# Optimization experiments

Hardware: AMD Instinct MI355X
Metric: run time of the kernel (lower is better)

## Reference

```python
import jax, jax.numpy as jnp
import numpy as np
import math

N = 8192
IN_FEATURES = 512
OUT_FEATURES = 512
BUCKET = 4          # self.bucket -> number of hash buckets
NHASH = 1           # nHashTable hardcoded to 1 in forward
NEG = -9e15         # sentinel used by the original module


def setup_inputs() -> dict:
    key = jax.random.key(0)
    k_in, k_adj, k_rot, k_kw, k_vw = jax.random.split(key, 5)
    inp = jax.random.normal(k_in, (N, IN_FEATURES), dtype=jnp.float32)
    adj = jax.random.randint(k_adj, (N, N), 0, 2, dtype=jnp.int32)
    rotations_rands = jax.random.normal(k_rot, (NHASH, OUT_FEATURES, BUCKET // 2), dtype=jnp.float32)
    # xavier_uniform with gain=1.414 for (in, out) matrices
    limit = 1.414 * math.sqrt(6.0 / (IN_FEATURES + OUT_FEATURES))
    kW = jax.random.uniform(k_kw, (IN_FEATURES, OUT_FEATURES), minval=-limit, maxval=limit, dtype=jnp.float32)
    vW = jax.random.uniform(k_vw, (IN_FEATURES, OUT_FEATURES), minval=-limit, maxval=limit, dtype=jnp.float32)
    return {"input": inp, "adj": adj, "rotations_rands": rotations_rands, "kW": kW, "vW": vW}


def reference(input, adj, rotations_rands, kW, vW):
    kh = input @ kW                      # [N, H]
    vh = input @ vW                      # [N, H]
    H = kh.shape[1]

    # LSH bucketing: rotate keys, argmax over [r, -r] -> bucket id per node
    rv = jnp.einsum('nh,thb->tnb', kh, rotations_rands)   # [1, N, B/2]
    rv = jnp.concatenate([rv, -rv], axis=-1)              # [1, N, B]
    buckets = jnp.argmax(rv, axis=2)[0]                   # [N]

    # Original scatters per-bucket kh@kh.T blocks into a dense NxN matrix
    # initialized at NEG; equivalent to masking full scores by same-bucket.
    same_bucket = buckets[:, None] == buckets[None, :]    # [N, N]
    scores = (kh @ kh.T) / jnp.sqrt(jnp.asarray(H, kh.dtype))
    K = jnp.where(same_bucket, scores, NEG)

    attention = jnp.where(adj > 0, K, NEG)
    attention = jax.nn.softmax(attention, axis=1)
    # dropout is identity in eval mode (reference runs in eval)
    h_prime = attention @ vh                              # [N, H]
    return jax.nn.elu(h_prime)                            # concat=True -> ELU
```

## Files before the change

kernel.cpp:

```cpp
#include <hip/hip_runtime.h>
#include <hip/hip_bf16.h>
#include <math.h>

#define N_NODES 8192
#define FEAT 512
#define NEGV -9e15f
#define VHPT_W 8704

typedef __attribute__((ext_vector_type(8))) short short8;
typedef __attribute__((ext_vector_type(4))) float floatx4;

#define OFF_KH    0UL
#define OFF_VH    16777216UL
#define OFF_KHP   33554432UL
#define OFF_VHPT  42074112UL
#define OFF_MASK  50987008UL
#define OFF_S     59375616UL
#define OFF_PERM  109707264UL
#define OFF_FLAGS 109740032UL
#define OFF_BUCK  109772800UL
#define OFF_META  109805568UL
#define OFF_CMEAN 109806592UL
#define WS_NEEDED 109808640UL
#define CAP_S     25165824L

#define OFF_AHI   (OFF_S)
#define OFF_ALO   (OFF_S + 8388608UL)
#define OFF_WKHI  (OFF_S + 16777216UL)
#define OFF_WKLO  (OFF_S + 17301504UL)
#define OFF_WVHI  (OFF_S + 17825792UL)
#define OFF_WVLO  (OFF_S + 18350080UL)
#define OFF_CW    (OFF_MASK)

static __device__ __forceinline__ unsigned short f2bf_bits(float x) {
  __hip_bfloat16 h = __float2bfloat16(x);
  unsigned short u;
  __builtin_memcpy(&u, &h, 2);
  return u;
}
static __device__ __forceinline__ float bf_bits2f(unsigned short u) {
  __hip_bfloat16 h;
  __builtin_memcpy(&h, &u, 2);
  return __bfloat162float(h);
}

static __device__ __forceinline__ void async_copy16(const void* gptr,
                                                    void* lptr) {
  __builtin_amdgcn_global_load_lds(
      (const __attribute__((address_space(1))) unsigned int*)gptr,
      (__attribute__((address_space(3))) unsigned int*)lptr, 16, 0, 0);
}

__global__ __launch_bounds__(256) void convert_input(
    const float* __restrict__ A, __hip_bfloat16* __restrict__ Ahi,
    __hip_bfloat16* __restrict__ Alo) {
  const long idx = ((long)blockIdx.x * 256 + threadIdx.x) * 4;
  const float4 v = *(const float4*)&A[idx];
  const float vv[4] = {v.x, v.y, v.z, v.w};
  ushort4 hi, lo;
  unsigned short* hp = (unsigned short*)&hi;
  unsigned short* lp = (unsigned short*)&lo;
#pragma unroll
  for (int e = 0; e < 4; e++) {
    unsigned short h = f2bf_bits(vv[e]);
    hp[e] = h;
    lp[e] = f2bf_bits(vv[e] - bf_bits2f(h));
  }
  *(ushort4*)&Ahi[idx] = hi;
  *(ushort4*)&Alo[idx] = lo;
}

__global__ __launch_bounds__(256) void convert_w(
    const float* __restrict__ kW, const float* __restrict__ vW,
    __hip_bfloat16* __restrict__ WkhiT, __hip_bfloat16* __restrict__ WkloT,
    __hip_bfloat16* __restrict__ WvhiT, __hip_bfloat16* __restrict__ WvloT) {
  __shared__ float tile[64][65];
  const int z = blockIdx.z;
  const float* __restrict__ W = z ? vW : kW;
  __hip_bfloat16* __restrict__ HiT = z ? WvhiT : WkhiT;
  __hip_bfloat16* __restrict__ LoT = z ? WvloT : WkloT;
  const int k0 = blockIdx.x * 64, n0 = blockIdx.y * 64;
  const int t = threadIdx.x;
#pragma unroll
  for (int s = 0; s < 16; s++) {
    int idx = t + s * 256;
    int r = idx >> 6, c = idx & 63;
    tile[r][c] = W[(long)(k0 + r) * FEAT + n0 + c];
  }
  __syncthreads();
#pragma unroll
  for (int s = 0; s < 16; s++) {
    int idx = t + s * 256;
    int a = idx >> 6, b = idx & 63;
    float w = tile[b][a];
    unsigned short h = f2bf_bits(w);
    unsigned short l = f2bf_bits(w - bf_bits2f(h));
    __builtin_memcpy(&HiT[(long)(n0 + a) * FEAT + k0 + b], &h, 2);
    __builtin_memcpy(&LoT[(long)(n0 + a) * FEAT + k0 + b], &l, 2);
  }
}

__global__ __launch_bounds__(256) void mfma_dual(
    const __hip_bfloat16* __restrict__ Ahi, const __hip_bfloat16* __restrict__ Alo,
    const __hip_bfloat16* __restrict__ WkhiT, const __hip_bfloat16* __restrict__ WkloT,
    const __hip_bfloat16* __restrict__ WvhiT, const __hip_bfloat16* __restrict__ WvloT,
    float* __restrict__ kh, float* __restrict__ vh) {
  const int z = blockIdx.z;
  const __hip_bfloat16* __restrict__ WhiT = z ? WvhiT : WkhiT;
  const __hip_bfloat16* __restrict__ WloT = z ? WvloT : WkloT;
  float* __restrict__ outp = z ? vh : kh;
  const int ti = blockIdx.x, tj = blockIdx.y;
  __shared__ __align__(16) __hip_bfloat16 Ah[128 * 32];
  __shared__ __align__(16) __hip_bfloat16 Al[128 * 32];
  __shared__ __align__(16) __hip_bfloat16 Wh[128 * 32];
  __shared__ __align__(16) __hip_bfloat16 Wl[128 * 32];
  const int t = threadIdx.x;
  const int lane = t & 63, w = t >> 6;
  const int wm = (w >> 1) * 64, wn = (w & 1) * 64;
  const int quad = lane >> 4, ln = lane & 15;
  const int qr = quad * 8;
  floatx4 acc[4][4];
#pragma unroll
  for (int mi = 0; mi < 4; mi++)
#pragma unroll
    for (int ni = 0; ni < 4; ni++) acc[mi][ni] = (floatx4)0.f;
  for (int k0 = 0; k0 < FEAT; k0 += 32) {
    __syncthreads();
#pragma unroll
    for (int s = 0; s < 2; s++) {
      int c = t + s * 256;
      int row = c >> 2, off8 = (c & 3) * 8;
      int lo = row * 32 + off8;
      async_copy16(&Ahi[(long)(ti * 128 + row) * FEAT + k0 + off8], &Ah[lo]);
      async_copy16(&Alo[(long)(ti * 128 + row) * FEAT + k0 + off8], &Al[lo]);
      async_copy16(&WhiT[(long)(tj * 128 + row) * FEAT + k0 + off8], &Wh[lo]);
      async_copy16(&WloT[(long)(tj * 128 + row) * FEAT + k0 + off8], &Wl[lo]);
    }
    __syncthreads();
    short8 ah[4], al[4], bh[4], bl[4];
#pragma unroll
    for (int mi = 0; mi < 4; mi++) {
      ah[mi] = *(const short8*)&Ah[(wm + mi * 16 + ln) * 32 + qr];
      al[mi] = *(const short8*)&Al[(wm + mi * 16 + ln) * 32 + qr];
    }
#pragma unroll
    for (int ni = 0; ni < 4; ni++) {
      bh[ni] = *(const short8*)&Wh[(wn + ni * 16 + ln) * 32 + qr];
      bl[ni] = *(const short8*)&Wl[(wn + ni * 16 + ln) * 32 + qr];
    }
#pragma unroll
    for (int mi = 0; mi < 4; mi++)
#pragma unroll
      for (int ni = 0; ni < 4; ni++) {
        acc[mi][ni] = __builtin_amdgcn_mfma_f32_16x16x32_bf16(
            ah[mi], bh[ni], acc[mi][ni], 0, 0, 0);
        acc[mi][ni] = __builtin_amdgcn_mfma_f32_16x16x32_bf16(
            ah[mi], bl[ni], acc[mi][ni], 0, 0, 0);
        acc[mi][ni] = __builtin_amdgcn_mfma_f32_16x16x32_bf16(
            al[mi], bh[ni], acc[mi][ni], 0, 0, 0);
      }
  }
#pragma unroll
  for (int mi = 0; mi < 4; mi++)
#pragma unroll
    for (int ni = 0; ni < 4; ni++) {
      int cc = tj * 128 + wn + ni * 16 + ln;
#pragma unroll
      for (int reg = 0; reg < 4; reg++) {
        int r = ti * 128 + wm + mi * 16 + quad * 4 + reg;
        outp[(long)r * FEAT + cc] = acc[mi][ni][reg];
      }
    }
}

__global__ __launch_bounds__(64) void cw_kernel(
    const float* __restrict__ kW, const float* __restrict__ rot,
    double* __restrict__ cw) {
  const int f = blockIdx.x;
  const int lane = threadIdx.x;
  double r0 = 0.0, r1 = 0.0;
  for (int h = lane; h < FEAT; h += 64) {
    double a = (double)kW[(long)f * FEAT + h];
    r0 += a * (double)rot[2 * h];
    r1 += a * (double)rot[2 * h + 1];
  }
#pragma unroll
  for (int off = 32; off > 0; off >>= 1) {
    r0 += __shfl_down(r0, off);
    r1 += __shfl_down(r1, off);
  }
  if (lane == 0) {
    cw[2 * f] = r0;
    cw[2 * f + 1] = r1;
  }
}

__global__ __launch_bounds__(64) void rv_bucket_kernel(
    const float* __restrict__ input, const double* __restrict__ cw,
    int* __restrict__ buckets) {
  const int i = blockIdx.x;
  const int lane = threadIdx.x;
  double r0 = 0.0, r1 = 0.0;
  for (int f = lane; f < FEAT; f += 64) {
    double a = (double)input[(long)i * FEAT + f];
    r0 += a * cw[2 * f];
    r1 += a * cw[2 * f + 1];
  }
#pragma unroll
  for (int off = 32; off > 0; off >>= 1) {
    r0 += __shfl_down(r0, off);
    r1 += __shfl_down(r1, off);
  }
  if (lane == 0) {
    int b = 0;
    double best = r0;
    if (r1 > best)  { best = r1;  b = 1; }
    if (-r0 > best) { best = -r0; b = 2; }
    if (-r1 > best) { best = -r1; b = 3; }
    buckets[i] = b;
  }
}

__global__ __launch_bounds__(256) void sort_kernel(
    const int* __restrict__ buckets, int* __restrict__ perm,
    int* __restrict__ meta, float* __restrict__ cmean) {
  __shared__ int lc[4][256];
  __shared__ int sc[4][256];
  __shared__ int boff_sh[5];
  const int t = threadIdx.x;
  cmean[t] = 0.f;
  cmean[t + 256] = 0.f;
  const int base = t * 32;
  int c0 = 0, c1 = 0, c2 = 0, c3 = 0;
  for (int k = 0; k < 32; k++) {
    int b = buckets[base + k];
    c0 += (b == 0); c1 += (b == 1); c2 += (b == 2); c3 += (b == 3);
  }
  lc[0][t] = c0; lc[1][t] = c1; lc[2][t] = c2; lc[3][t] = c3;
  sc[0][t] = c0; sc[1][t] = c1; sc[2][t] = c2; sc[3][t] = c3;
  __syncthreads();
  for (int off = 1; off < 256; off <<= 1) {
    int a0 = (t >= off) ? sc[0][t - off] : 0;
    int a1 = (t >= off) ? sc[1][t - off] : 0;
    int a2 = (t >= off) ? sc[2][t - off] : 0;
    int a3 = (t >= off) ? sc[3][t - off] : 0;
    __syncthreads();
    sc[0][t] += a0; sc[1][t] += a1; sc[2][t] += a2; sc[3][t] += a3;
    __syncthreads();
  }
  if (t == 0) {
    int boff[5];
    boff[0] = 0;
    for (int b = 0; b < 4; b++) boff[b + 1] = boff[b] + sc[b][255];
    for (int b = 0; b < 5; b++) { meta[b] = boff[b]; boff_sh[b] = boff[b]; }
    long so = 0;
    int po = 0;
    for (int b = 0; b < 4; b++) {
      int tot = boff[b + 1] - boff[b];
      int pad = ((tot + 127) >> 7) << 7;
      meta[5 + b] = pad;
      meta[9 + b] = (int)so;
      meta[14 + b] = po;
      so += (long)pad * pad;
      po += pad;
    }
    meta[13] = (int)so;
    meta[18] = po;
    if (so > CAP_S)
      for (int b = 0; b < 4; b++) meta[5 + b] = 0;
  }
  __syncthreads();
  int s0 = boff_sh[0] + sc[0][t] - lc[0][t];
  int s1 = boff_sh[1] + sc[1][t] - lc[1][t];
  int s2 = boff_sh[2] + sc[2][t] - lc[2][t];
  int s3 = boff_sh[3] + sc[3][t] - lc[3][t];
  for (int k = 0; k < 32; k++) {
    int i = base + k;
    int b = buckets[i];
    int pos = (b == 0) ? s0++ : ((b == 1) ? s1++ : ((b == 2) ? s2++ : s3++));
    perm[pos] = i;
  }
}

__global__ __launch_bounds__(256) void gather_khp_kernel(
    const float* __restrict__ kh, const int* __restrict__ perm,
    __hip_bfloat16* __restrict__ khp) {
  const int g = blockIdx.x;
  const int t = threadIdx.x;
  if (g < N_NODES) {
    const int p = perm[g];
    const float2 v = *(const float2*)&kh[(long)p * FEAT + 2 * t];
    khp[(long)g * FEAT + 2 * t] = __float2bfloat16(v.x);
    khp[(long)g * FEAT + 2 * t + 1] = __float2bfloat16(v.y);
  } else {
    khp[(long)g * FEAT + 2 * t] = __float2bfloat16(0.f);
    khp[(long)g * FEAT + 2 * t + 1] = __float2bfloat16(0.f);
  }
}

__global__ __launch_bounds__(256) void transpose_vhpT_kernel(
    const float* __restrict__ vh, const int* __restrict__ perm,
    const int* __restrict__ meta, __hip_bfloat16* __restrict__ vhpT,
    float* __restrict__ cmean) {
  __shared__ float tile[64][65];
  __shared__ float cred[4][64];
  const int g0 = blockIdx.x * 64;
  const int f0 = blockIdx.y * 64;
  const int t = threadIdx.x;
#pragma unroll
  for (int s = 0; s < 16; s++) {
    int idx = t + s * 256;
    int r = idx >> 6, c = idx & 63;
    int pos = g0 + r;
    int b = (pos >= meta[15]) + (pos >= meta[16]) + (pos >= meta[17]);
    int local = pos - meta[14 + b];
    int n_b = meta[b + 1] - meta[b];
    float v = 0.f;
    if (local < n_b) v = vh[(long)perm[meta[b] + local] * FEAT + f0 + c];
    tile[r][c] = v;
  }
  __syncthreads();
  {
    const int c = t & 63, seg = t >> 6;
    float ps = 0.f;
#pragma unroll
    for (int rr = 0; rr < 16; rr++) ps += tile[seg * 16 + rr][c];
    cred[seg][c] = ps;
  }
  __syncthreads();
  if (t < 64)
    atomicAdd(&cmean[f0 + t],
              cred[0][t] + cred[1][t] + cred[2][t] + cred[3][t]);
#pragma unroll
  for (int s = 0; s < 16; s++) {
    int idx = t + s * 256;
    int fr = idx >> 6, gc = idx & 63;
    vhpT[(long)(f0 + fr) * VHPT_W + g0 + gc] = __float2bfloat16(tile[gc][fr]);
  }
}

__global__ __launch_bounds__(256) void maskpack_kernel(
    const int* __restrict__ adj, const int* __restrict__ perm,
    const int* __restrict__ meta, unsigned long long* __restrict__ maskbits) {
  __shared__ int adj_lds[N_NODES];
  const int g = blockIdx.x;
  const int t = threadIdx.x;
  const int b = (g >= meta[1]) + (g >= meta[2]) + (g >= meta[3]);
  const int boff = meta[b];
  const int n_b = meta[b + 1] - boff;
  const int padded = meta[5 + b];
  const int i = perm[g];
  const int* arow = adj + (long)i * N_NODES;
#pragma unroll
  for (int s = 0; s < 8; s++) {
    int idx = (t + s * 256) * 4;
    *(int4*)&adj_lds[idx] = *(const int4*)&arow[idx];
  }
  __syncthreads();
  const int lane = t & 63, w = t >> 6;
  for (int jj0 = w * 64; jj0 < padded; jj0 += 256) {
    int jj = jj0 + lane;
    int pred = 0;
    if (jj < n_b) pred = adj_lds[perm[boff + jj]] > 0;
    unsigned long long mword = __ballot(pred);
    if (lane == 0) maskbits[(long)g * 128 + (jj0 >> 6)] = mword;
  }
}

__global__ __launch_bounds__(256) void s_gemm(
    const __hip_bfloat16* __restrict__ khp, const int* __restrict__ meta,
    const unsigned long long* __restrict__ maskbits,
    __hip_bfloat16* __restrict__ S) {
  const int b = blockIdx.z;
  const int padded = meta[5 + b];
  const int ti = blockIdx.x, tj = blockIdx.y;
  if (ti * 128 >= padded || tj * 128 >= padded) return;
  const int boff = meta[b];
  const long soff = meta[9 + b];
  __shared__ __align__(16) __hip_bfloat16 As[128 * 32];
  __shared__ __align__(16) __hip_bfloat16 Bs[128 * 32];
  const int t = threadIdx.x;
  const int lane = t & 63, w = t >> 6;
  const int wm = (w >> 1) * 64, wn = (w & 1) * 64;
  const int quad = lane >> 4, ln = lane & 15;
  const int qr = quad * 8;
  floatx4 acc[4][4];
#pragma unroll
  for (int mi = 0; mi < 4; mi++)
#pragma unroll
    for (int ni = 0; ni < 4; ni++) acc[mi][ni] = (floatx4)0.f;
  const long a_g0 = boff + ti * 128;
  const long b_g0 = boff + tj * 128;
  for (int k0 = 0; k0 < FEAT; k0 += 32) {
    __syncthreads();
#pragma unroll
    for (int s = 0; s < 2; s++) {
      int c = t + s * 256;
      int row = c >> 2, off8 = (c & 3) * 8;
      int lo = row * 32 + off8;
      async_copy16(&khp[(a_g0 + row) * FEAT + k0 + off8], &As[lo]);
      async_copy16(&khp[(b_g0 + row) * FEAT + k0 + off8], &Bs[lo]);
    }
    __syncthreads();
    short8 af[4], bfr[4];
#pragma unroll
    for (int mi = 0; mi < 4; mi++)
      af[mi] = *(const short8*)&As[(wm + mi * 16 + ln) * 32 + qr];
#pragma unroll
    for (int ni = 0; ni < 4; ni++)
      bfr[ni] = *(const short8*)&Bs[(wn + ni * 16 + ln) * 32 + qr];
#pragma unroll
    for (int mi = 0; mi < 4; mi++)
#pragma unroll
      for (int ni = 0; ni < 4; ni++)
        acc[mi][ni] = __builtin_amdgcn_mfma_f32_16x16x32_bf16(
            af[mi], bfr[ni], acc[mi][ni], 0, 0, 0);
  }
  const float scale = 0.04419417382415922f;
#pragma unroll
  for (int mi = 0; mi < 4; mi++) {
#pragma unroll
    for (int ni = 0; ni < 4; ni++) {
      int cb = tj * 128 + wn + ni * 16;
#pragma unroll
      for (int reg = 0; reg < 4; reg++) {
        int r = ti * 128 + wm + mi * 16 + quad * 4 + reg;
        unsigned long long wbits = maskbits[(long)(boff + r) * 128 + (cb >> 6)];
        int bit = (int)((wbits >> ((cb & 63) + ln)) & 1ULL);
        float v = acc[mi][ni][reg] * scale;
        S[soff + (long)r * padded + cb + ln] =
            __float2bfloat16(bit ? v : NEGV);
      }
    }
  }
}

__global__ __launch_bounds__(256) void softmax_kernel(
    __hip_bfloat16* __restrict__ S, const int* __restrict__ meta,
    int* __restrict__ flags) {
  const int g = blockIdx.x;
  const int b = (g >= meta[1]) + (g >= meta[2]) + (g >= meta[3]);
  const int boff = meta[b];
  const int padded = meta[5 + b];
  const long soff = meta[9 + b];
  __hip_bfloat16* row = S + soff + (long)(g - boff) * padded;
  __shared__ float red[256];
  __shared__ float pb[8192];
  const int t = threadIdx.x;
  float m = -INFINITY;
  for (int j0 = t * 8; j0 < padded; j0 += 2048) {
    union { short8 v; unsigned short u[8]; } pk;
    pk.v = *(const short8*)&row[j0];
#pragma unroll
    for (int e = 0; e < 8; e++) {
      float s = bf_bits2f(pk.u[e]);
      pb[j0 + e] = s;
      m = fmaxf(m, s);
    }
  }
  red[t] = m;
  __syncthreads();
#pragma unroll
  for (int o = 128; o > 0; o >>= 1) {
    if (t < o) red[t] = fmaxf(red[t], red[t + o]);
    __syncthreads();
  }
  m = red[0];
  __syncthreads();
  if (m < -8e15f) {
    if (t == 0) flags[g] = 1;
    union { short8 v; unsigned short u[8]; } zz;
#pragma unroll
    for (int e = 0; e < 8; e++) zz.u[e] = 0;
    for (int j0 = t * 8; j0 < padded; j0 += 2048) *(short8*)&row[j0] = zz.v;
    return;
  }
  if (t == 0) flags[g] = 0;
  float sum = 0.f;
  for (int j0 = t * 8; j0 < padded; j0 += 2048) {
#pragma unroll
    for (int e = 0; e < 8; e++) {
      float ex = expf(pb[j0 + e] - m);
      pb[j0 + e] = ex;
      sum += ex;
    }
  }
  red[t] = sum;
  __syncthreads();
#pragma unroll
  for (int o = 128; o > 0; o >>= 1) {
    if (t < o) red[t] += red[t + o];
    __syncthreads();
  }
  const float inv = 1.f / red[0];
  for (int j0 = t * 8; j0 < padded; j0 += 2048) {
    union { short8 v; unsigned short u[8]; } pk;
#pragma unroll
    for (int e = 0; e < 8; e++) pk.u[e] = f2bf_bits(pb[j0 + e] * inv);
    *(short8*)&row[j0] = pk.v;
  }
}

__global__ __launch_bounds__(256) void pv_gemm(
    const __hip_bfloat16* __restrict__ S, const __hip_bfloat16* __restrict__ vhpT,
    const int* __restrict__ meta, const int* __restrict__ perm,
    const int* __restrict__ flags, const float* __restrict__ cmean,
    float* __restrict__ out) {
  const int b = blockIdx.z;
  const int padded = meta[5 + b];
  const int ti = blockIdx.x;
  if (ti * 128 >= padded) return;
  const int boff = meta[b];
  const int n_b = meta[b + 1] - boff;
  const long soff = meta[9 + b];
  const int poff = meta[14 + b];
  const int f0 = blockIdx.y * 64;
  __shared__ __align__(16) __hip_bfloat16 As[128 * 32];
  __shared__ __align__(16) __hip_bfloat16 Bs[64 * 32];
  const int t = threadIdx.x;
  const int lane = t & 63, w = t >> 6;
  const int wm = w * 32;
  const int quad = lane >> 4, ln = lane & 15;
  const int qr = quad * 8;
  floatx4 acc[2][4];
#pragma unroll
  for (int mi = 0; mi < 2; mi++)
#pragma unroll
    for (int ni = 0; ni < 4; ni++) acc[mi][ni] = (floatx4)0.f;
  const long r0 = (long)ti * 128;
  for (int k0 = 0; k0 < padded; k0 += 32) {
    __syncthreads();
#pragma unroll
    for (int s = 0; s < 2; s++) {
      int c = t + s * 256;
      int row = c >> 2, off8 = (c & 3) * 8;
      async_copy16(&S[soff + (r0 + row) * padded + k0 + off8],
                   &As[row * 32 + off8]);
    }
    {
      int row = t >> 2, off8 = (t & 3) * 8;
      async_copy16(&vhpT[(long)(f0 + row) * VHPT_W + poff + k0 + off8],
                   &Bs[row * 32 + off8]);
    }
    __syncthreads();
    short8 af[2], bfr[4];
#pragma unroll
    for (int mi = 0; mi < 2; mi++)
      af[mi] = *(const short8*)&As[(wm + mi * 16 + ln) * 32 + qr];
#pragma unroll
    for (int ni = 0; ni < 4; ni++)
      bfr[ni] = *(const short8*)&Bs[(ni * 16 + ln) * 32 + qr];
#pragma unroll
    for (int mi = 0; mi < 2; mi++)
#pragma unroll
      for (int ni = 0; ni < 4; ni++)
        acc[mi][ni] = __builtin_amdgcn_mfma_f32_16x16x32_bf16(
            af[mi], bfr[ni], acc[mi][ni], 0, 0, 0);
  }
#pragma unroll
  for (int mi = 0; mi < 2; mi++) {
#pragma unroll
    for (int reg = 0; reg < 4; reg++) {
      int r = ti * 128 + wm + mi * 16 + quad * 4 + reg;
      if (r < n_b) {
        int g = boff + r;
        int node = perm[g];
        int fl = flags[g];
#pragma unroll
        for (int ni = 0; ni < 4; ni++) {
          int fc = f0 + ni * 16 + ln;
          float v = fl ? cmean[fc] * (1.f / (float)N_NODES)
                       : acc[mi][ni][reg];
          v = v > 0.f ? v : expm1f(v);
          out[(long)node * FEAT + fc] = v;
        }
      }
    }
  }
}

__global__ __launch_bounds__(256) void gemm_dual(
    const float* __restrict__ A, const float* __restrict__ Wk,
    const float* __restrict__ Wv, float* __restrict__ kh,
    float* __restrict__ vh) {
  __shared__ float As[32][33];
  __shared__ float Bk[32][33];
  __shared__ float Bv[32][33];
  const int tid = threadIdx.x;
  const int row0 = blockIdx.x * 32;
  const int col0 = blockIdx.y * 32;
  const int tx = tid & 15, ty = tid >> 4;
  float ck00 = 0.f, ck01 = 0.f, ck10 = 0.f, ck11 = 0.f;
  float cv00 = 0.f, cv01 = 0.f, cv10 = 0.f, cv11 = 0.f;
  for (int kt = 0; kt < FEAT; kt += 32) {
#pragma unroll
    for (int t = 0; t < 4; t++) {
      int e = tid + t * 256;
      int r = e >> 5, c = e & 31;
      As[r][c] = A[(long)(row0 + r) * FEAT + kt + c];
      Bk[r][c] = Wk[(long)(kt + r) * FEAT + col0 + c];
      Bv[r][c] = Wv[(long)(kt + r) * FEAT + col0 + c];
    }
    __syncthreads();
#pragma unroll
    for (int kk = 0; kk < 32; kk++) {
      float a0 = As[ty * 2][kk], a1 = As[ty * 2 + 1][kk];
      float bk0 = Bk[kk][tx * 2], bk1 = Bk[kk][tx * 2 + 1];
      float bv0 = Bv[kk][tx * 2], bv1 = Bv[kk][tx * 2 + 1];
      ck00 += a0 * bk0; ck01 += a0 * bk1;
      ck10 += a1 * bk0; ck11 += a1 * bk1;
      cv00 += a0 * bv0; cv01 += a0 * bv1;
      cv10 += a1 * bv0; cv11 += a1 * bv1;
    }
    __syncthreads();
  }
  const int r0 = row0 + ty * 2, c0 = col0 + tx * 2;
  kh[(long)r0 * FEAT + c0] = ck00;       kh[(long)r0 * FEAT + c0 + 1] = ck01;
  kh[(long)(r0 + 1) * FEAT + c0] = ck10; kh[(long)(r0 + 1) * FEAT + c0 + 1] = ck11;
  vh[(long)r0 * FEAT + c0] = cv00;       vh[(long)r0 * FEAT + c0 + 1] = cv01;
  vh[(long)(r0 + 1) * FEAT + c0] = cv10; vh[(long)(r0 + 1) * FEAT + c0 + 1] = cv11;
}

__global__ __launch_bounds__(64) void bucket_kernel(
    const float* __restrict__ kh, const float* __restrict__ rot,
    int* __restrict__ buckets) {
  const int i = blockIdx.x;
  const int lane = threadIdx.x;
  double r0 = 0.0, r1 = 0.0;
  for (int h = lane; h < FEAT; h += 64) {
    double a = (double)kh[(long)i * FEAT + h];
    r0 += a * (double)rot[2 * h];
    r1 += a * (double)rot[2 * h + 1];
  }
#pragma unroll
  for (int off = 32; off > 0; off >>= 1) {
    r0 += __shfl_down(r0, off);
    r1 += __shfl_down(r1, off);
  }
  if (lane == 0) {
    int b = 0;
    double best = r0;
    if (r1 > best)  { best = r1;  b = 1; }
    if (-r0 > best) { best = -r0; b = 2; }
    if (-r1 > best) { best = -r1; b = 3; }
    buckets[i] = b;
  }
}

__global__ __launch_bounds__(256) void attn_kernel(
    const float* __restrict__ kh, const float* __restrict__ vh,
    const int* __restrict__ adj, const int* __restrict__ buckets,
    float* __restrict__ out) {
  __shared__ float khi[FEAT];
  __shared__ float pbuf[N_NODES];
  __shared__ unsigned short jlist[N_NODES];
  __shared__ int cnt_sh;
  __shared__ float red[256];
  const int i = blockIdx.x;
  const int tid = threadIdx.x;
  if (tid == 0) cnt_sh = 0;
  for (int k = tid; k < FEAT; k += 256) khi[k] = kh[(long)i * FEAT + k];
  const int mybucket = buckets[i];
  __syncthreads();
  const int* adjrow = adj + (long)i * N_NODES;
  for (int j = tid; j < N_NODES; j += 256) {
    if (adjrow[j] > 0 && buckets[j] == mybucket) {
      int idx = atomicAdd(&cnt_sh, 1);
      jlist[idx] = (unsigned short)j;
    }
  }
  __syncthreads();
  const int cnt = cnt_sh;
  float mloc = -INFINITY;
  for (int idx = tid; idx < cnt; idx += 256) {
    int j = jlist[idx];
    const float4* kj = (const float4*)(kh + (long)j * FEAT);
    const float4* ki = (const float4*)khi;
    float acc = 0.f;
#pragma unroll 8
    for (int k = 0; k < FEAT / 4; k++) {
      float4 a = ki[k];
      float4 b = kj[k];
      acc += a.x * b.x + a.y * b.y + a.z * b.z + a.w * b.w;
    }
    float s = acc * 0.04419417382415922f;
    pbuf[idx] = s;
    mloc = fmaxf(mloc, s);
  }
  red[tid] = mloc;
  __syncthreads();
#pragma unroll
  for (int off = 128; off > 0; off >>= 1) {
    if (tid < off) red[tid] = fmaxf(red[tid], red[tid + off]);
    __syncthreads();
  }
  const float m = red[0];
  __syncthreads();
  float lloc = 0.f;
  for (int idx = tid; idx < cnt; idx += 256) {
    float p = expf(pbuf[idx] - m);
    pbuf[idx] = p;
    lloc += p;
  }
  red[tid] = lloc;
  __syncthreads();
#pragma unroll
  for (int off = 128; off > 0; off >>= 1) {
    if (tid < off) red[tid] += red[tid + off];
    __syncthreads();
  }
  const float l = red[0];
  __syncthreads();
  const int f = 2 * tid;
  float acc0 = 0.f, acc1 = 0.f;
  if (cnt > 0) {
#pragma unroll 4
    for (int idx = 0; idx < cnt; idx++) {
      int j = jlist[idx];
      float p = pbuf[idx];
      float2 v = *(const float2*)(vh + (long)j * FEAT + f);
      acc0 += p * v.x;
      acc1 += p * v.y;
    }
    float invl = 1.f / l;
    acc0 *= invl;
    acc1 *= invl;
  } else {
    for (int j = 0; j < N_NODES; j++) {
      float2 v = *(const float2*)(vh + (long)j * FEAT + f);
      acc0 += v.x;
      acc1 += v.y;
    }
    acc0 *= (1.f / (float)N_NODES);
    acc1 *= (1.f / (float)N_NODES);
  }
  acc0 = acc0 > 0.f ? acc0 : expm1f(acc0);
  acc1 = acc1 > 0.f ? acc1 : expm1f(acc1);
  *(float2*)(out + (long)i * FEAT + f) = make_float2(acc0, acc1);
}

extern "C" void kernel_launch(void* const* d_in, const int* in_sizes, int n_in,
                              void* d_out, int out_size, void* d_ws,
                              size_t ws_size, hipStream_t stream) {
  const float* input = (const float*)d_in[0];
  const int* adj = (const int*)d_in[1];
  const float* rot = (const float*)d_in[2];
  const float* kW = (const float*)d_in[3];
  const float* vW = (const float*)d_in[4];
  float* out = (float*)d_out;

  char* ws = (char*)d_ws;

  if (ws_size >= WS_NEEDED) {
    float* kh = (float*)(ws + OFF_KH);
    float* vh = (float*)(ws + OFF_VH);
    __hip_bfloat16* khp = (__hip_bfloat16*)(ws + OFF_KHP);
    __hip_bfloat16* vhpT = (__hip_bfloat16*)(ws + OFF_VHPT);
    unsigned long long* maskbits = (unsigned long long*)(ws + OFF_MASK);
    __hip_bfloat16* S = (__hip_bfloat16*)(ws + OFF_S);
    int* perm = (int*)(ws + OFF_PERM);
    int* flags = (int*)(ws + OFF_FLAGS);
    int* buckets = (int*)(ws + OFF_BUCK);
    int* meta = (int*)(ws + OFF_META);
    float* cmean = (float*)(ws + OFF_CMEAN);
    __hip_bfloat16* Ahi = (__hip_bfloat16*)(ws + OFF_AHI);
    __hip_bfloat16* Alo = (__hip_bfloat16*)(ws + OFF_ALO);
    __hip_bfloat16* WkhiT = (__hip_bfloat16*)(ws + OFF_WKHI);
    __hip_bfloat16* WkloT = (__hip_bfloat16*)(ws + OFF_WKLO);
    __hip_bfloat16* WvhiT = (__hip_bfloat16*)(ws + OFF_WVHI);
    __hip_bfloat16* WvloT = (__hip_bfloat16*)(ws + OFF_WVLO);
    double* cw = (double*)(ws + OFF_CW);

    convert_input<<<4096, 256, 0, stream>>>(input, Ahi, Alo);
    convert_w<<<dim3(8, 8, 2), 256, 0, stream>>>(kW, vW, WkhiT, WkloT, WvhiT,
                                                 WvloT);
    mfma_dual<<<dim3(64, 4, 2), 256, 0, stream>>>(Ahi, Alo, WkhiT, WkloT,
                                                  WvhiT, WvloT, kh, vh);
    cw_kernel<<<512, 64, 0, stream>>>(kW, rot, cw);
    rv_bucket_kernel<<<N_NODES, 64, 0, stream>>>(input, cw, buckets);
    sort_kernel<<<1, 256, 0, stream>>>(buckets, perm, meta, cmean);
    gather_khp_kernel<<<N_NODES + 128, 256, 0, stream>>>(kh, perm, khp);
    transpose_vhpT_kernel<<<dim3(VHPT_W / 64, FEAT / 64), 256, 0, stream>>>(
        vh, perm, meta, vhpT, cmean);
    maskpack_kernel<<<N_NODES, 256, 0, stream>>>(adj, perm, meta, maskbits);
    s_gemm<<<dim3(64, 64, 4), 256, 0, stream>>>(khp, meta, maskbits, S);
    softmax_kernel<<<N_NODES, 256, 0, stream>>>(S, meta, flags);
    pv_gemm<<<dim3(64, 8, 4), 256, 0, stream>>>(S, vhpT, meta, perm, flags,
                                                cmean, out);
  } else {
    float* kh = (float*)(ws + 0UL);
    float* vh = (float*)(ws + 16777216UL);
    int* buckets = (int*)(ws + 33554432UL);
    dim3 gemm_grid(N_NODES / 32, FEAT / 32);
    gemm_dual<<<gemm_grid, 256, 0, stream>>>(input, kW, vW, kh, vh);
    bucket_kernel<<<N_NODES, 64, 0, stream>>>(kh, rot, buckets);
    attn_kernel<<<N_NODES, 256, 0, stream>>>(kh, vh, adj, buckets, out);
  }
}
```

Before: 648.9 us.

## Exploit symmetry of kh·khᵀ in bucket score GEMM and stage output through LDS

The per-bucket score GEMM now computes only upper-triangular 128x128 tiles, since kh·khᵀ is symmetric, and writes each tile plus its transpose to S. The output is staged through padded shared memory so the mask is applied and stores go out as 16-byte vectors instead of scalar bf16 writes. This roughly halves the MFMA work and khp loads for the score stage. In exchange it adds a transposed LDS read pass with possible bank conflicts and makes the off-diagonal blocks do twice the store work.

```diff
diff --git a/kernel.cpp b/kernel.cpp
--- a/kernel.cpp
+++ b/kernel.cpp
@@ -374,11 +374,12 @@
   const int b = blockIdx.z;
   const int padded = meta[5 + b];
   const int ti = blockIdx.x, tj = blockIdx.y;
-  if (ti * 128 >= padded || tj * 128 >= padded) return;
+  if (ti * 128 >= padded || tj * 128 >= padded || tj < ti) return;
   const int boff = meta[b];
   const long soff = meta[9 + b];
-  __shared__ __align__(16) __hip_bfloat16 As[128 * 32];
-  __shared__ __align__(16) __hip_bfloat16 Bs[128 * 32];
+  __shared__ __align__(16) __hip_bfloat16 smem[128 * 136];
+  __hip_bfloat16* As = smem;
+  __hip_bfloat16* Bs = smem + 128 * 32;
   const int t = threadIdx.x;
   const int lane = t & 63, w = t >> 6;
   const int wm = (w >> 1) * 64, wn = (w & 1) * 64;
@@ -417,20 +418,53 @@
             af[mi], bfr[ni], acc[mi][ni], 0, 0, 0);
   }
   const float scale = 0.04419417382415922f;
-#pragma unroll
-  for (int mi = 0; mi < 4; mi++) {
+  __syncthreads();
+  __hip_bfloat16* Ct = smem;
+#pragma unroll
+  for (int mi = 0; mi < 4; mi++)
 #pragma unroll
     for (int ni = 0; ni < 4; ni++) {
-      int cb = tj * 128 + wn + ni * 16;
+      int col = wn + ni * 16 + ln;
 #pragma unroll
       for (int reg = 0; reg < 4; reg++) {
-        int r = ti * 128 + wm + mi * 16 + quad * 4 + reg;
-        unsigned long long wbits = maskbits[(long)(boff + r) * 128 + (cb >> 6)];
-        int bit = (int)((wbits >> ((cb & 63) + ln)) & 1ULL);
-        float v = acc[mi][ni][reg] * scale;
-        S[soff + (long)r * padded + cb + ln] =
-            __float2bfloat16(bit ? v : NEGV);
+        int row = wm + mi * 16 + quad * 4 + reg;
+        Ct[row * 136 + col] = __float2bfloat16(acc[mi][ni][reg] * scale);
       }
+    }
+  __syncthreads();
+  const unsigned short negb = f2bf_bits(NEGV);
+#pragma unroll
+  for (int i = 0; i < 8; i++) {
+    int idx = t + i * 256;
+    int rl = idx >> 4, c8 = (idx & 15) * 8;
+    int rg = ti * 128 + rl;
+    int cg = tj * 128 + c8;
+    union { short8 v; unsigned short u[8]; } pk;
+    pk.v = *(const short8*)&Ct[rl * 136 + c8];
+    unsigned long long wbits = maskbits[(long)(boff + rg) * 128 + (cg >> 6)];
+#pragma unroll
+    for (int e = 0; e < 8; e++)
+      if (!((wbits >> ((cg & 63) + e)) & 1ULL)) pk.u[e] = negb;
+    *(short8*)&S[soff + (long)rg * padded + cg] = pk.v;
+  }
+  if (ti != tj) {
+#pragma unroll
+    for (int i = 0; i < 8; i++) {
+      int idx = t + i * 256;
+      int cl = idx >> 4, r8 = (idx & 15) * 8;
+      int rg = tj * 128 + cl;
+      int cg = ti * 128 + r8;
+      union { short8 v; unsigned short u[8]; } pk;
+#pragma unroll
+      for (int e = 0; e < 8; e++) {
+        __hip_bfloat16 hv = Ct[(r8 + e) * 136 + cl];
+        __builtin_memcpy(&pk.u[e], &hv, 2);
+      }
+      unsigned long long wbits = maskbits[(long)(boff + rg) * 128 + (cg >> 6)];
+#pragma unroll
+      for (int e = 0; e < 8; e++)
+        if (!((wbits >> ((cg & 63) + e)) & 1ULL)) pk.u[e] = negb;
+      *(short8*)&S[soff + (long)rg * padded + cg] = pk.v;
     }
   }
 }
```

After: 645.6 us. About the same (-0.5%).
